# Performance work log

Hardware: AMD Instinct MI355X
Metric: run time of the kernel (lower is better)

## Reference

```python
import jax, jax.numpy as jnp
import numpy as np

N_NODES = 50000
N_EDGES = 1600000


def setup_inputs() -> dict:
    key = jax.random.key(0)
    ks = jax.random.split(key, 12)
    x = jax.random.normal(ks[0], (N_NODES, 128), dtype=jnp.float32)
    edge_index = jax.random.randint(ks[1], (2, N_EDGES), 0, N_NODES, dtype=jnp.int32)
    edge_weight = jax.random.uniform(ks[2], (N_EDGES,), dtype=jnp.float32)
    K = 3
    def glorot(k, kk, cin, cout):
        s = (6.0 / (cin + cout)) ** 0.5
        return jax.random.uniform(k, (kk, cin, cout), dtype=jnp.float32, minval=-s, maxval=s)
    W0 = glorot(ks[3], K, 128, 128); b0 = jnp.zeros((128,), jnp.float32)
    W1 = glorot(ks[4], K, 128, 128); b1 = jnp.zeros((128,), jnp.float32)
    W2 = glorot(ks[5], K, 128, 64);  b2 = jnp.zeros((64,), jnp.float32)
    return {"x": x, "edge_index": edge_index, "edge_weight": edge_weight,
            "W0": W0, "b0": b0, "W1": W1, "b1": b1, "W2": W2, "b2": b2}


def _laplacian_norm(edge_index, edge_weight, n_nodes):
    # PyG ChebConv with lambda_max=2.0, sym normalization:
    # L_hat = 2*(I - D^-1/2 A D^-1/2)/lambda_max - I = -D^-1/2 A D^-1/2 (zero diag)
    src, dst = edge_index[0], edge_index[1]
    deg = jax.ops.segment_sum(edge_weight, src, num_segments=n_nodes)
    dinv = jnp.where(deg > 0, jax.lax.rsqrt(jnp.maximum(deg, 1e-30)), 0.0)
    return -dinv[src] * edge_weight * dinv[dst]


def _spmm(norm, src, dst, x, n_nodes):
    # out[i] = sum_{e: dst[e]=i} norm[e] * x[src[e]]
    return jax.ops.segment_sum(norm[:, None] * x[src], dst, num_segments=n_nodes)


def _cheb_conv(x, src, dst, norm, W, b, n_nodes):
    K = W.shape[0]
    out = jnp.einsum('nc,cd->nd', x, W[0])
    tx0 = x
    tx1 = _spmm(norm, src, dst, x, n_nodes)  # L_hat @ x
    out = out + jnp.einsum('nc,cd->nd', tx1, W[1])
    for k in range(2, K):
        tx2 = 2.0 * _spmm(norm, src, dst, tx1, n_nodes) - tx0
        out = out + jnp.einsum('nc,cd->nd', tx2, W[k])
        tx0, tx1 = tx1, tx2
    return out + b


def reference(x, edge_index, edge_weight, W0, b0, W1, b1, W2, b2):
    n_nodes = x.shape[0]
    src, dst = edge_index[0], edge_index[1]
    norm = _laplacian_norm(edge_index, edge_weight, n_nodes)
    h = jax.nn.sigmoid(_cheb_conv(x, src, dst, norm, W0, b0, n_nodes))
    h = jax.nn.sigmoid(_cheb_conv(h, src, dst, norm, W1, b1, n_nodes))
    return jax.nn.sigmoid(_cheb_conv(h, src, dst, norm, W2, b2, n_nodes))
```

## Files before the change

### kernel.cpp

```cpp
#include <hip/hip_runtime.h>
#include <hip/hip_fp16.h>
#include <math.h>

#define N_NODES 50000
#define N_EDGES 1600000
#define NBUCK 196
#define EBLK 400
#define CHUNK 4000
#define CSR_CAP (N_EDGES + 2048 * NBUCK + 4096)

typedef _Float16 f16x8 __attribute__((ext_vector_type(8)));
typedef _Float16 f16x4 __attribute__((ext_vector_type(4)));
typedef _Float16 f16x2 __attribute__((ext_vector_type(2)));
typedef float f32x4 __attribute__((ext_vector_type(4)));
typedef float f32x2 __attribute__((ext_vector_type(2)));

union HBits { __half h; unsigned short u; };

__global__ __launch_bounds__(256) void k_bcount(const int* __restrict__ src,
                                                const int* __restrict__ dst,
                                                int* __restrict__ bcnt_d,
                                                int* __restrict__ bcnt_s) {
    __shared__ int lcd[256];
    __shared__ int lcs[256];
    int tid = threadIdx.x;
    lcd[tid] = 0; lcs[tid] = 0;
    __syncthreads();
    int base = blockIdx.x * CHUNK;
    for (int i = tid; i < CHUNK; i += 256) {
        atomicAdd(&lcd[dst[base + i] >> 8], 1);
        atomicAdd(&lcs[src[base + i] >> 8], 1);
    }
    __syncthreads();
    bcnt_d[blockIdx.x * 256 + tid] = lcd[tid];
    bcnt_s[blockIdx.x * 256 + tid] = lcs[tid];
}

__global__ __launch_bounds__(256) void k_bscan1(int* __restrict__ bcnt_d,
                                                int* __restrict__ bcnt_s,
                                                int* __restrict__ btot) {
    int b = blockIdx.x & 255;
    int* bcnt = (blockIdx.x >> 8) ? bcnt_s : bcnt_d;
    int tid = threadIdx.x;
    int k0 = 2 * tid;
    int v0 = (k0 < EBLK) ? bcnt[k0 * 256 + b] : 0;
    int v1 = (k0 + 1 < EBLK) ? bcnt[(k0 + 1) * 256 + b] : 0;
    int pair = v0 + v1;
    __shared__ int s[256];
    s[tid] = pair;
    __syncthreads();
    for (int off = 1; off < 256; off <<= 1) {
        int t = (tid >= off) ? s[tid - off] : 0;
        __syncthreads();
        s[tid] += t;
        __syncthreads();
    }
    int excl = s[tid] - pair;
    if (k0 < EBLK)     bcnt[k0 * 256 + b] = excl;
    if (k0 + 1 < EBLK) bcnt[(k0 + 1) * 256 + b] = excl + v0;
    if (tid == 255) btot[(blockIdx.x >> 8) * 256 + b] = s[255];
}

__global__ __launch_bounds__(256) void k_bscan2(const int* __restrict__ btot,
                                                int* __restrict__ bstart_d,
                                                int* __restrict__ bstart_s) {
    __shared__ int s[256];
    int b = threadIdx.x;
    int v = btot[b];
    s[b] = v;
    __syncthreads();
    for (int off = 1; off < 256; off <<= 1) {
        int t = (b >= off) ? s[b - off] : 0;
        __syncthreads();
        s[b] += t;
        __syncthreads();
    }
    bstart_d[b] = s[b] - v;
    if (b == 0) bstart_d[256] = N_EDGES;
    __syncthreads();
    int v2 = btot[256 + b];
    s[b] = v2;
    __syncthreads();
    for (int off = 1; off < 256; off <<= 1) {
        int t = (b >= off) ? s[b - off] : 0;
        __syncthreads();
        s[b] += t;
        __syncthreads();
    }
    bstart_s[b] = s[b] - v2;
    if (b == 0) bstart_s[256] = N_EDGES;
}

__global__ __launch_bounds__(256) void k_bscatter(const int* __restrict__ src,
                                                  const int* __restrict__ dst,
                                                  const float* __restrict__ w,
                                                  const int* __restrict__ bcnt_d,
                                                  const int* __restrict__ bcnt_s,
                                                  const int* __restrict__ bstart_d,
                                                  const int* __restrict__ bstart_s,
                                                  uint2* __restrict__ dsw,
                                                  unsigned* __restrict__ ssw) {
    __shared__ int curd[256];
    __shared__ int curs[256];
    int tid = threadIdx.x;
    curd[tid] = bcnt_d[blockIdx.x * 256 + tid] + bstart_d[tid];
    curs[tid] = bcnt_s[blockIdx.x * 256 + tid] + bstart_s[tid];
    __syncthreads();
    int base = blockIdx.x * CHUNK;
    for (int i = tid; i < CHUNK; i += 256) {
        int d = dst[base + i];
        int ss = src[base + i];
        float wi = w[base + i];
        int p = atomicAdd(&curd[d >> 8], 1);
        uint2 r; r.x = (unsigned)ss | ((unsigned)(d & 255) << 16);
        r.y = __float_as_uint(wi);
        dsw[p] = r;
        int q = atomicAdd(&curs[ss >> 8], 1);
        HBits hw; hw.h = __float2half(wi);
        ssw[q] = (unsigned)(ss & 255) | ((unsigned)hw.u << 16);
    }
}

__global__ __launch_bounds__(256) void k_sdeg(const unsigned* __restrict__ ssw,
                                              const int* __restrict__ bstart_s,
                                              float* __restrict__ dinv) {
    __shared__ float h[256];
    int tid = threadIdx.x;
    int b = blockIdx.x;
    h[tid] = 0.f;
    __syncthreads();
    int e0 = bstart_s[b], e1 = bstart_s[b + 1];
    for (int i = e0 + tid; i < e1; i += 256) {
        unsigned r = ssw[i];
        HBits hb; hb.u = (unsigned short)(r >> 16);
        atomicAdd(&h[r & 255], __half2float(hb.h));
    }
    __syncthreads();
    int node = (b << 8) + tid;
    if (node < N_NODES) {
        float d = h[tid];
        dinv[node] = d > 0.f ? rsqrtf(fmaxf(d, 1e-30f)) : 0.f;
    }
}

__global__ __launch_bounds__(256) void k_bcsr(const uint2* __restrict__ dsw,
                                              const int* __restrict__ bstart_d,
                                              const float* __restrict__ dinv,
                                              uint2* __restrict__ ri,
                                              unsigned* __restrict__ csr4) {
    __shared__ int ncnt[256];
    __shared__ int cur[256];
    __shared__ int sc[256];
    __shared__ float ldinv[256];
    int tid = threadIdx.x;
    int b = blockIdx.x;
    int node = (b << 8) + tid;
    ncnt[tid] = 0;
    ldinv[tid] = (node < N_NODES) ? dinv[node] : 0.f;
    __syncthreads();
    int e0 = bstart_d[b], e1 = bstart_d[b + 1];
    for (int i = e0 + tid; i < e1; i += 256)
        atomicAdd(&ncnt[(dsw[i].x >> 16) & 255], 1);
    __syncthreads();
    int v = ncnt[tid];
    int pc = (v + 7) & ~7;
    sc[tid] = pc;
    __syncthreads();
    for (int off = 1; off < 256; off <<= 1) {
        int t = (tid >= off) ? sc[tid - off] : 0;
        __syncthreads();
        sc[tid] += t;
        __syncthreads();
    }
    int excl = sc[tid] - pc;
    cur[tid] = excl;
    int pbase = ((e0 + 7) & ~7) + 2048 * b;
    if (node < N_NODES) {
        uint2 r; r.x = (unsigned)(pbase + excl); r.y = (unsigned)pc;
        ri[node] = r;
    }
    __syncthreads();
    for (int i = e0 + tid; i < e1; i += 256) {
        uint2 sw = dsw[i];
        int srcn = sw.x & 0xFFFF;
        int ld = (sw.x >> 16) & 255;
        int p = pbase + atomicAdd(&cur[ld], 1);
        float nv = -dinv[srcn] * __uint_as_float(sw.y) * ldinv[ld];
        HBits hb; hb.h = __float2half(nv);
        csr4[p] = (unsigned)srcn | ((unsigned)hb.u << 16);
    }
    __syncthreads();
    int st = pbase + excl;
    for (int i = v; i < pc; i++) csr4[st + i] = 0u;
}

__device__ inline void wt_one(const float* __restrict__ W, __half* __restrict__ Wt,
                              int C, int i) {
    int n = i >> 7, k = i & 127;
    int slice = n / C, c = n % C;
    float v;
    if (slice == 0)      v = 2.f * W[(size_t)(256 + k) * C + c];
    else if (slice == 1) v = W[(size_t)(128 + k) * C + c];
    else                 v = W[(size_t)k * C + c] - W[(size_t)(256 + k) * C + c];
    Wt[i] = __float2half(v);
}

__global__ __launch_bounds__(256) void k_prep(const float* __restrict__ x,
                                              __half* __restrict__ X,
                                              const float* __restrict__ W0,
                                              const float* __restrict__ W1,
                                              const float* __restrict__ W2,
                                              __half* __restrict__ Wt0,
                                              __half* __restrict__ Wt1,
                                              __half* __restrict__ Wt2) {
    int bid = blockIdx.x, tid = threadIdx.x;
    if (bid < 6250) {
        int i = bid * 256 + tid;
        float4 v = *(const float4*)&x[(size_t)i * 4];
        f16x4 o;
        o[0] = (_Float16)v.x; o[1] = (_Float16)v.y;
        o[2] = (_Float16)v.z; o[3] = (_Float16)v.w;
        *(f16x4*)&X[(size_t)i * 4] = o;
    } else if (bid < 6250 + 192) {
        wt_one(W0, Wt0, 128, (bid - 6250) * 256 + tid);
    } else if (bid < 6250 + 384) {
        wt_one(W1, Wt1, 128, (bid - 6250 - 192) * 256 + tid);
    } else {
        wt_one(W2, Wt2, 64, (bid - 6250 - 384) * 256 + tid);
    }
}

__device__ inline void mac_pair(const __half* __restrict__ Tbase, unsigned ea,
                                unsigned eb, int stin, float acc[8]) {
    f16x8 r0 = *(const f16x8*)&Tbase[(size_t)(ea & 0xFFFFu) * stin];
    f16x8 r1 = *(const f16x8*)&Tbase[(size_t)(eb & 0xFFFFu) * stin];
    unsigned np = (ea >> 16) | (eb & 0xFFFF0000u);
    f16x2 nv; __builtin_memcpy(&nv, &np, 4);
    #pragma unroll
    for (int f = 0; f < 8; f++) {
        f16x2 h; h[0] = r0[f]; h[1] = r1[f];
        acc[f] = __builtin_amdgcn_fdot2(h, nv, acc[f], false);
    }
}

__device__ inline void macv_f8(uint2 v, unsigned ce, float acc[8]) {
    HBits hb; hb.u = (unsigned short)(ce >> 16);
    float n = __half2float(hb.h);
    f32x2 p0 = __builtin_amdgcn_cvt_pk_f32_fp8(v.x, false);
    f32x2 p1 = __builtin_amdgcn_cvt_pk_f32_fp8(v.x, true);
    f32x2 p2 = __builtin_amdgcn_cvt_pk_f32_fp8(v.y, false);
    f32x2 p3 = __builtin_amdgcn_cvt_pk_f32_fp8(v.y, true);
    acc[0] = fmaf(n, p0[0], acc[0]);
    acc[1] = fmaf(n, p0[1], acc[1]);
    acc[2] = fmaf(n, p1[0], acc[2]);
    acc[3] = fmaf(n, p1[1], acc[3]);
    acc[4] = fmaf(n, p2[0], acc[4]);
    acc[5] = fmaf(n, p2[1], acc[5]);
    acc[6] = fmaf(n, p3[0], acc[6]);
    acc[7] = fmaf(n, p3[1], acc[7]);
}

__device__ inline void mac_e8(const unsigned char* __restrict__ Tb, unsigned ce,
                              int stin, float acc[8]) {
    uint2 v = *(const uint2*)&Tb[(size_t)(ce & 0xFFFFu) * (size_t)stin];
    macv_f8(v, ce, acc);
}

template <int ST_IN, int ST_ADD, int ST_OUT, int FW, int SIG, int F32, int GF8,
          int F8OUT>
__global__ __launch_bounds__(256) void k_spmm(const void* __restrict__ Xin,
                                              const __half* __restrict__ Add,
                                              void* __restrict__ outp,
                                              const float* __restrict__ bias,
                                              const uint2* __restrict__ ri,
                                              const unsigned* __restrict__ csr4) {
    constexpr int NL = FW / 8;
    constexpr int EG = 64 / NL;
    int node = blockIdx.x * 4 + (threadIdx.x >> 6);
    int lane = threadIdx.x & 63;
    int eg = lane / NL;
    int fs = lane % NL;
    uint2 rv = ri[node];
    int s = (int)rv.x;
    int e = s + (int)rv.y;
    const __half* Tbase = (const __half*)Xin + fs * 8;
    const unsigned char* Tb8 = (const unsigned char*)Xin + fs * 8;
    float acc[8];
    #pragma unroll
    for (int f = 0; f < 8; f++) acc[f] = 0.f;

    int j = s;
    if (GF8) {
        if (EG == 4) {
            for (; j + 32 <= e; j += 32) {
                uint4 c0 = *(const uint4*)&csr4[j + 4 * eg];
                uint4 c1 = *(const uint4*)&csr4[j + 16 + 4 * eg];
                unsigned ce[8] = {c0.x, c0.y, c0.z, c0.w, c1.x, c1.y, c1.z, c1.w};
                uint2 g[8];
                #pragma unroll
                for (int k = 0; k < 8; k++)
                    g[k] = *(const uint2*)&Tb8[(size_t)(ce[k] & 0xFFFFu) * (size_t)ST_IN];
                #pragma unroll
                for (int k = 0; k < 8; k++) macv_f8(g[k], ce[k], acc);
            }
            if (j + 16 <= e) {
                uint4 c0 = *(const uint4*)&csr4[j + 4 * eg];
                unsigned ce[4] = {c0.x, c0.y, c0.z, c0.w};
                uint2 g[4];
                #pragma unroll
                for (int k = 0; k < 4; k++)
                    g[k] = *(const uint2*)&Tb8[(size_t)(ce[k] & 0xFFFFu) * (size_t)ST_IN];
                #pragma unroll
                for (int k = 0; k < 4; k++) macv_f8(g[k], ce[k], acc);
                j += 16;
            }
            if (j + 8 <= e) {
                uint2 c = *(const uint2*)&csr4[j + 2 * eg];
                mac_e8(Tb8, c.x, ST_IN, acc);
                mac_e8(Tb8, c.y, ST_IN, acc);
            }
        } else {
            for (; j + 32 <= e; j += 32) {
                uint4 c0 = *(const uint4*)&csr4[j + 4 * eg];
                unsigned ce[4] = {c0.x, c0.y, c0.z, c0.w};
                uint2 g[4];
                #pragma unroll
                for (int k = 0; k < 4; k++)
                    g[k] = *(const uint2*)&Tb8[(size_t)(ce[k] & 0xFFFFu) * (size_t)ST_IN];
                #pragma unroll
                for (int k = 0; k < 4; k++) macv_f8(g[k], ce[k], acc);
            }
            if (j + 16 <= e) {
                uint2 c = *(const uint2*)&csr4[j + 2 * eg];
                mac_e8(Tb8, c.x, ST_IN, acc);
                mac_e8(Tb8, c.y, ST_IN, acc);
                j += 16;
            }
            if (j + 8 <= e) {
                uint2 c = *(const uint2*)&csr4[j + 2 * (eg & 3)];
                unsigned ea = c.x, eb = c.y;
                if (eg >= 4) { ea &= 0xFFFFu; eb &= 0xFFFFu; }
                mac_e8(Tb8, ea, ST_IN, acc);
                mac_e8(Tb8, eb, ST_IN, acc);
            }
        }
    } else if (EG == 4) {
        for (; j + 32 <= e; j += 32) {
            uint4 c0 = *(const uint4*)&csr4[j + 4 * eg];
            uint4 c1 = *(const uint4*)&csr4[j + 16 + 4 * eg];
            unsigned ea[4] = {c0.x, c0.z, c1.x, c1.z};
            unsigned eb[4] = {c0.y, c0.w, c1.y, c1.w};
            f16x8 r0[4], r1[4];
            #pragma unroll
            for (int k = 0; k < 4; k++) {
                r0[k] = *(const f16x8*)&Tbase[(size_t)(ea[k] & 0xFFFFu) * ST_IN];
                r1[k] = *(const f16x8*)&Tbase[(size_t)(eb[k] & 0xFFFFu) * ST_IN];
            }
            #pragma unroll
            for (int k = 0; k < 4; k++) {
                unsigned np = (ea[k] >> 16) | (eb[k] & 0xFFFF0000u);
                f16x2 nv; __builtin_memcpy(&nv, &np, 4);
                #pragma unroll
                for (int f = 0; f < 8; f++) {
                    f16x2 h; h[0] = r0[k][f]; h[1] = r1[k][f];
                    acc[f] = __builtin_amdgcn_fdot2(h, nv, acc[f], false);
                }
            }
        }
        if (j + 16 <= e) {
            uint4 c0 = *(const uint4*)&csr4[j + 4 * eg];
            mac_pair(Tbase, c0.x, c0.y, ST_IN, acc);
            mac_pair(Tbase, c0.z, c0.w, ST_IN, acc);
            j += 16;
        }
        if (j + 8 <= e) {
            uint2 c = *(const uint2*)&csr4[j + 2 * eg];
            mac_pair(Tbase, c.x, c.y, ST_IN, acc);
        }
    } else {
        for (; j + 32 <= e; j += 32) {
            uint4 c0 = *(const uint4*)&csr4[j + 4 * eg];
            unsigned ea[2] = {c0.x, c0.z};
            unsigned eb[2] = {c0.y, c0.w};
            f16x8 r0[2], r1[2];
            #pragma unroll
            for (int k = 0; k < 2; k++) {
                r0[k] = *(const f16x8*)&Tbase[(size_t)(ea[k] & 0xFFFFu) * ST_IN];
                r1[k] = *(const f16x8*)&Tbase[(size_t)(eb[k] & 0xFFFFu) * ST_IN];
            }
            #pragma unroll
            for (int k = 0; k < 2; k++) {
                unsigned np = (ea[k] >> 16) | (eb[k] & 0xFFFF0000u);
                f16x2 nv; __builtin_memcpy(&nv, &np, 4);
                #pragma unroll
                for (int f = 0; f < 8; f++) {
                    f16x2 h; h[0] = r0[k][f]; h[1] = r1[k][f];
                    acc[f] = __builtin_amdgcn_fdot2(h, nv, acc[f], false);
                }
            }
        }
        if (j + 16 <= e) {
            uint2 c = *(const uint2*)&csr4[j + 2 * eg];
            mac_pair(Tbase, c.x, c.y, ST_IN, acc);
            j += 16;
        }
        if (j + 8 <= e) {
            uint2 c = *(const uint2*)&csr4[j + 2 * (eg & 3)];
            unsigned ea = c.x, eb = c.y;
            if (eg >= 4) { ea &= 0xFFFFu; eb &= 0xFFFFu; }
            mac_pair(Tbase, ea, eb, ST_IN, acc);
        }
    }
    #pragma unroll
    for (int f = 0; f < 8; f++)
        for (int m = NL; m < 64; m <<= 1)
            acc[f] += __shfl_xor(acc[f], m);
    if (eg == 0) {
        f16x8 av = *(const f16x8*)&Add[(size_t)node * ST_ADD + fs * 8];
        float v[8];
        #pragma unroll
        for (int f = 0; f < 8; f++) v[f] = acc[f] + (float)av[f];
        if (SIG) {
            #pragma unroll
            for (int f = 0; f < 8; f++) {
                v[f] += bias[fs * 8 + f];
                v[f] = 1.f / (1.f + expf(-v[f]));
            }
        }
        if (F32) {
            float* o = (float*)outp + (size_t)node * ST_OUT + fs * 8;
            float4 o0; o0.x = v[0]; o0.y = v[1]; o0.z = v[2]; o0.w = v[3];
            float4 o1; o1.x = v[4]; o1.y = v[5]; o1.z = v[6]; o1.w = v[7];
            *(float4*)&o[0] = o0;
            *(float4*)&o[4] = o1;
        } else if (F8OUT) {
            int w0 = __builtin_amdgcn_cvt_pk_fp8_f32(v[0], v[1], 0, false);
            w0 = __builtin_amdgcn_cvt_pk_fp8_f32(v[2], v[3], w0, true);
            int w1 = __builtin_amdgcn_cvt_pk_fp8_f32(v[4], v[5], 0, false);
            w1 = __builtin_amdgcn_cvt_pk_fp8_f32(v[6], v[7], w1, true);
            uint2 o; o.x = (unsigned)w0; o.y = (unsigned)w1;
            *(uint2*)((unsigned char*)outp + (size_t)node * ST_OUT + fs * 8) = o;
        } else {
            f16x8 o;
            #pragma unroll
            for (int f = 0; f < 8; f++) o[f] = (_Float16)v[f];
            *(f16x8*)((__half*)outp + (size_t)node * ST_OUT + fs * 8) = o;
        }
    }
}

template <int CC, int STG>
__global__ __launch_bounds__(256) void k_gemm(const __half* __restrict__ A,
                                              const __half* __restrict__ Wt,
                                              __half* __restrict__ G,
                                              unsigned char* __restrict__ P8,
                                              int M) {
    constexpr int N3 = 3 * CC;
    constexpr int NF = N3 / 16;
    constexpr int NP = CC / 16;
    __shared__ _Float16 As[64][40];
    __shared__ _Float16 Bs[N3][40];
    int tid = threadIdx.x;
    int wave = tid >> 6, lane = tid & 63;
    int lm = lane & 15, lq = lane >> 4;
    int m0 = blockIdx.x * 64;
    f32x4 acc[NF];
    for (int nf = 0; nf < NF; nf++) acc[nf] = (f32x4)0.0f;

    for (int k0 = 0; k0 < 128; k0 += 32) {
        {
            int r = tid >> 2, q = tid & 3;
            int row = m0 + r;
            if (row >= M) row = M - 1;
            *(f16x8*)&As[r][q * 8] = *(const f16x8*)&A[(size_t)row * 128 + k0 + q * 8];
        }
        for (int i = 0; i < N3 / 64; i++) {
            int idx = tid + i * 256;
            int n = idx >> 2, q = idx & 3;
            *(f16x8*)&Bs[n][q * 8] = *(const f16x8*)&Wt[(size_t)n * 128 + k0 + q * 8];
        }
        __syncthreads();
        f16x8 a = *(const f16x8*)&As[wave * 16 + lm][lq * 8];
        for (int nf = 0; nf < NF; nf++) {
            f16x8 b = *(const f16x8*)&Bs[nf * 16 + lm][lq * 8];
            acc[nf] = __builtin_amdgcn_mfma_f32_16x16x32_f16(a, b, acc[nf], 0, 0, 0);
        }
        __syncthreads();
    }
    for (int nf = 0; nf < NF; nf++) {
        for (int r = 0; r < 4; r++) {
            int grow = m0 + wave * 16 + lq * 4 + r;
            int col = nf * 16 + lm;
            if (grow < M) {
                if (nf < NP) {
                    int pk = __builtin_amdgcn_cvt_pk_fp8_f32(acc[nf][r], acc[nf][r],
                                                             0, false);
                    P8[(size_t)grow * CC + col] = (unsigned char)(pk & 0xFF);
                } else {
                    G[(size_t)grow * STG + (col - CC)] = __float2half(acc[nf][r]);
                }
            }
        }
    }
}

extern "C" void kernel_launch(void* const* d_in, const int* in_sizes, int n_in,
                              void* d_out, int out_size, void* d_ws, size_t ws_size,
                              hipStream_t stream) {
    const float* x  = (const float*)d_in[0];
    const int*   ei = (const int*)d_in[1];
    const float* ew = (const float*)d_in[2];
    const float* W0 = (const float*)d_in[3];
    const float* b0 = (const float*)d_in[4];
    const float* W1 = (const float*)d_in[5];
    const float* b1 = (const float*)d_in[6];
    const float* W2 = (const float*)d_in[7];
    const float* b2 = (const float*)d_in[8];
    const int* src = ei;
    const int* dst = ei + N_EDGES;

    char* ws = (char*)d_ws;
    size_t off = 0;
    auto alloc = [&](size_t bytes) -> char* {
        size_t p = (off + 255) & ~(size_t)255;
        off = p + bytes;
        return ws + p;
    };
    __half*   X      = (__half*)alloc((size_t)N_NODES * 128 * 2);
    __half*   G      = (__half*)alloc((size_t)N_NODES * 256 * 2);
    __half*   TMP    = (__half*)alloc((size_t)N_NODES * 128 * 2);
    unsigned char* P8 = (unsigned char*)alloc((size_t)N_NODES * 128);
    unsigned char* TMP8 = (unsigned char*)alloc((size_t)N_NODES * 128);
    unsigned* csr4   = (unsigned*)alloc((size_t)CSR_CAP * 4);
    uint2*    ri     = (uint2*)alloc((size_t)N_NODES * 8);
    uint2*    dsw    = (uint2*)alloc((size_t)N_EDGES * 8);
    unsigned* ssw    = (unsigned*)alloc((size_t)N_EDGES * 4);
    int*      bcnt_d = (int*)alloc((size_t)EBLK * 256 * 4);
    int*      bcnt_s = (int*)alloc((size_t)EBLK * 256 * 4);
    int*      btot   = (int*)alloc(512 * 4);
    int*      bstart_d = (int*)alloc(257 * 4);
    int*      bstart_s = (int*)alloc(257 * 4);
    float*    dinv   = (float*)alloc((size_t)N_NODES * 4);
    __half*   Wt0    = (__half*)alloc((size_t)384 * 128 * 2);
    __half*   Wt1    = (__half*)alloc((size_t)384 * 128 * 2);
    __half*   Wt2    = (__half*)alloc((size_t)192 * 128 * 2);

    k_bcount<<<EBLK, 256, 0, stream>>>(src, dst, bcnt_d, bcnt_s);
    k_bscan1<<<512, 256, 0, stream>>>(bcnt_d, bcnt_s, btot);
    k_bscan2<<<1, 256, 0, stream>>>(btot, bstart_d, bstart_s);
    k_bscatter<<<EBLK, 256, 0, stream>>>(src, dst, ew, bcnt_d, bcnt_s,
                                         bstart_d, bstart_s, dsw, ssw);
    k_sdeg<<<NBUCK, 256, 0, stream>>>(ssw, bstart_s, dinv);
    k_bcsr<<<NBUCK, 256, 0, stream>>>(dsw, bstart_d, dinv, ri, csr4);

    k_prep<<<6250 + 192 + 192 + 96, 256, 0, stream>>>(x, X, W0, W1, W2, Wt0, Wt1, Wt2);

    int gb = (N_NODES + 63) / 64;
    int sb = N_NODES / 4;
    k_gemm<128, 256><<<gb, 256, 0, stream>>>(X, Wt0, G, P8, N_NODES);
    k_spmm<128, 256, 128, 128, 0, 0, 1, 1><<<sb, 256, 0, stream>>>(P8, G, TMP8,
                                                                   nullptr, ri, csr4);
    k_spmm<128, 256, 128, 128, 1, 0, 1, 0><<<sb, 256, 0, stream>>>(TMP8, G + 128, X,
                                                                   b0, ri, csr4);
    k_gemm<128, 256><<<gb, 256, 0, stream>>>(X, Wt1, G, P8, N_NODES);
    k_spmm<128, 256, 128, 128, 0, 0, 1, 1><<<sb, 256, 0, stream>>>(P8, G, TMP8,
                                                                   nullptr, ri, csr4);
    k_spmm<128, 256, 128, 128, 1, 0, 1, 0><<<sb, 256, 0, stream>>>(TMP8, G + 128, X,
                                                                   b1, ri, csr4);
    k_gemm<64, 128><<<gb, 256, 0, stream>>>(X, Wt2, G, P8, N_NODES);
    k_spmm<64, 128, 64, 64, 0, 0, 1, 0><<<sb, 256, 0, stream>>>(P8, G, TMP,
                                                                nullptr, ri, csr4);
    k_spmm<64, 128, 64, 64, 1, 1, 0, 0><<<sb, 256, 0, stream>>>(TMP, G + 64, d_out,
                                                                b2, ri, csr4);
}
```

Before: 413.0 us.

## Stage bucket scatter in LDS and widen fp8 SpMM gathers to 16 bytes

The bucket scatter kernel now computes local per-bucket offsets with a block-level histogram and prefix scan. It stages records in shared memory and then writes them to global memory in contiguous runs, replacing scattered per-edge global writes. Separately, the 128-wide fp8 SpMM path now has each lane gather 16 bytes (16 features) per edge instead of 8, halving lanes per row and doubling edge groups. This adds LDS usage (about 48KB per block), which may limit occupancy, and extra passes over the input chunk.

```diff
diff --git a/kernel.cpp b/kernel.cpp
--- a/kernel.cpp
+++ b/kernel.cpp
@@ -100,24 +100,58 @@
                                                   const int* __restrict__ bstart_s,
                                                   uint2* __restrict__ dsw,
                                                   unsigned* __restrict__ ssw) {
-    __shared__ int curd[256];
-    __shared__ int curs[256];
+    __shared__ uint2 sbufd[CHUNK];
+    __shared__ unsigned sbufs[CHUNK];
+    __shared__ int lcd[256];
+    __shared__ int lcs[256];
+    __shared__ int curd_l[256];
+    __shared__ int curs_l[256];
+    __shared__ int gbase_d[256];
+    __shared__ int gbase_s[256];
     int tid = threadIdx.x;
-    curd[tid] = bcnt_d[blockIdx.x * 256 + tid] + bstart_d[tid];
-    curs[tid] = bcnt_s[blockIdx.x * 256 + tid] + bstart_s[tid];
+    lcd[tid] = 0; lcs[tid] = 0;
     __syncthreads();
     int base = blockIdx.x * CHUNK;
+    for (int i = tid; i < CHUNK; i += 256) {
+        atomicAdd(&lcd[dst[base + i] >> 8], 1);
+        atomicAdd(&lcs[src[base + i] >> 8], 1);
+    }
+    __syncthreads();
+    int vd = lcd[tid], vs = lcs[tid];
+    for (int off = 1; off < 256; off <<= 1) {
+        int td = (tid >= off) ? lcd[tid - off] : 0;
+        int ts = (tid >= off) ? lcs[tid - off] : 0;
+        __syncthreads();
+        lcd[tid] += td; lcs[tid] += ts;
+        __syncthreads();
+    }
+    int exd = lcd[tid] - vd, exs = lcs[tid] - vs;
+    curd_l[tid] = exd;
+    curs_l[tid] = exs;
+    gbase_d[tid] = bcnt_d[blockIdx.x * 256 + tid] + bstart_d[tid] - exd;
+    gbase_s[tid] = bcnt_s[blockIdx.x * 256 + tid] + bstart_s[tid] - exs;
+    __syncthreads();
     for (int i = tid; i < CHUNK; i += 256) {
         int d = dst[base + i];
         int ss = src[base + i];
         float wi = w[base + i];
-        int p = atomicAdd(&curd[d >> 8], 1);
-        uint2 r; r.x = (unsigned)ss | ((unsigned)(d & 255) << 16);
+        int p = atomicAdd(&curd_l[d >> 8], 1);
+        uint2 r;
+        r.x = (unsigned)ss | ((unsigned)(d & 255) << 16) | ((unsigned)(d >> 8) << 24);
         r.y = __float_as_uint(wi);
-        dsw[p] = r;
-        int q = atomicAdd(&curs[ss >> 8], 1);
+        sbufd[p] = r;
+        int q = atomicAdd(&curs_l[ss >> 8], 1);
         HBits hw; hw.h = __float2half(wi);
-        ssw[q] = (unsigned)(ss & 255) | ((unsigned)hw.u << 16);
+        sbufs[q] = (unsigned)ss | ((unsigned)hw.u << 16);
+    }
+    __syncthreads();
+    for (int i = tid; i < CHUNK; i += 256) {
+        uint2 r = sbufd[i];
+        dsw[gbase_d[(r.x >> 24) & 255] + i] = r;
+    }
+    for (int i = tid; i < CHUNK; i += 256) {
+        unsigned rs = sbufs[i];
+        ssw[gbase_s[(rs >> 8) & 255] + i] = rs;
     }
 }
 
@@ -266,6 +300,28 @@
     macv_f8(v, ce, acc);
 }
 
+__device__ inline void macv_f8q(uint4 v, unsigned ce, float acc[16]) {
+    HBits hb; hb.u = (unsigned short)(ce >> 16);
+    float n = __half2float(hb.h);
+    f32x2 p;
+    p = __builtin_amdgcn_cvt_pk_f32_fp8(v.x, false);
+    acc[0] = fmaf(n, p[0], acc[0]);  acc[1] = fmaf(n, p[1], acc[1]);
+    p = __builtin_amdgcn_cvt_pk_f32_fp8(v.x, true);
+    acc[2] = fmaf(n, p[0], acc[2]);  acc[3] = fmaf(n, p[1], acc[3]);
+    p = __builtin_amdgcn_cvt_pk_f32_fp8(v.y, false);
+    acc[4] = fmaf(n, p[0], acc[4]);  acc[5] = fmaf(n, p[1], acc[5]);
+    p = __builtin_amdgcn_cvt_pk_f32_fp8(v.y, true);
+    acc[6] = fmaf(n, p[0], acc[6]);  acc[7] = fmaf(n, p[1], acc[7]);
+    p = __builtin_amdgcn_cvt_pk_f32_fp8(v.z, false);
+    acc[8] = fmaf(n, p[0], acc[8]);  acc[9] = fmaf(n, p[1], acc[9]);
+    p = __builtin_amdgcn_cvt_pk_f32_fp8(v.z, true);
+    acc[10] = fmaf(n, p[0], acc[10]); acc[11] = fmaf(n, p[1], acc[11]);
+    p = __builtin_amdgcn_cvt_pk_f32_fp8(v.w, false);
+    acc[12] = fmaf(n, p[0], acc[12]); acc[13] = fmaf(n, p[1], acc[13]);
+    p = __builtin_amdgcn_cvt_pk_f32_fp8(v.w, true);
+    acc[14] = fmaf(n, p[0], acc[14]); acc[15] = fmaf(n, p[1], acc[15]);
+}
+
 template <int ST_IN, int ST_ADD, int ST_OUT, int FW, int SIG, int F32, int GF8,
           int F8OUT>
 __global__ __launch_bounds__(256) void k_spmm(const void* __restrict__ Xin,
@@ -274,7 +330,8 @@
                                               const float* __restrict__ bias,
                                               const uint2* __restrict__ ri,
                                               const unsigned* __restrict__ csr4) {
-    constexpr int NL = FW / 8;
+    constexpr int FPL = (GF8 && FW == 128) ? 16 : 8;
+    constexpr int NL = FW / FPL;
     constexpr int EG = 64 / NL;
     int node = blockIdx.x * 4 + (threadIdx.x >> 6);
     int lane = threadIdx.x & 63;
@@ -284,65 +341,59 @@
     int s = (int)rv.x;
     int e = s + (int)rv.y;
     const __half* Tbase = (const __half*)Xin + fs * 8;
-    const unsigned char* Tb8 = (const unsigned char*)Xin + fs * 8;
-    float acc[8];
+    const unsigned char* Tb8 = (const unsigned char*)Xin + fs * FPL;
+    float acc[FPL];
     #pragma unroll
-    for (int f = 0; f < 8; f++) acc[f] = 0.f;
+    for (int f = 0; f < FPL; f++) acc[f] = 0.f;
 
     int j = s;
-    if (GF8) {
-        if (EG == 4) {
-            for (; j + 32 <= e; j += 32) {
-                uint4 c0 = *(const uint4*)&csr4[j + 4 * eg];
-                uint4 c1 = *(const uint4*)&csr4[j + 16 + 4 * eg];
-                unsigned ce[8] = {c0.x, c0.y, c0.z, c0.w, c1.x, c1.y, c1.z, c1.w};
-                uint2 g[8];
-                #pragma unroll
-                for (int k = 0; k < 8; k++)
-                    g[k] = *(const uint2*)&Tb8[(size_t)(ce[k] & 0xFFFFu) * (size_t)ST_IN];
-                #pragma unroll
-                for (int k = 0; k < 8; k++) macv_f8(g[k], ce[k], acc);
-            }
-            if (j + 16 <= e) {
-                uint4 c0 = *(const uint4*)&csr4[j + 4 * eg];
-                unsigned ce[4] = {c0.x, c0.y, c0.z, c0.w};
-                uint2 g[4];
-                #pragma unroll
-                for (int k = 0; k < 4; k++)
-                    g[k] = *(const uint2*)&Tb8[(size_t)(ce[k] & 0xFFFFu) * (size_t)ST_IN];
-                #pragma unroll
-                for (int k = 0; k < 4; k++) macv_f8(g[k], ce[k], acc);
-                j += 16;
-            }
-            if (j + 8 <= e) {
-                uint2 c = *(const uint2*)&csr4[j + 2 * eg];
-                mac_e8(Tb8, c.x, ST_IN, acc);
-                mac_e8(Tb8, c.y, ST_IN, acc);
-            }
-        } else {
-            for (; j + 32 <= e; j += 32) {
-                uint4 c0 = *(const uint4*)&csr4[j + 4 * eg];
-                unsigned ce[4] = {c0.x, c0.y, c0.z, c0.w};
-                uint2 g[4];
-                #pragma unroll
-                for (int k = 0; k < 4; k++)
-                    g[k] = *(const uint2*)&Tb8[(size_t)(ce[k] & 0xFFFFu) * (size_t)ST_IN];
-                #pragma unroll
-                for (int k = 0; k < 4; k++) macv_f8(g[k], ce[k], acc);
-            }
-            if (j + 16 <= e) {
-                uint2 c = *(const uint2*)&csr4[j + 2 * eg];
-                mac_e8(Tb8, c.x, ST_IN, acc);
-                mac_e8(Tb8, c.y, ST_IN, acc);
-                j += 16;
-            }
-            if (j + 8 <= e) {
-                uint2 c = *(const uint2*)&csr4[j + 2 * (eg & 3)];
-                unsigned ea = c.x, eb = c.y;
-                if (eg >= 4) { ea &= 0xFFFFu; eb &= 0xFFFFu; }
-                mac_e8(Tb8, ea, ST_IN, acc);
-                mac_e8(Tb8, eb, ST_IN, acc);
-            }
+    if (GF8 && FW == 128) {
+        for (; j + 32 <= e; j += 32) {
+            uint4 c0 = *(const uint4*)&csr4[j + 4 * eg];
+            unsigned ce[4] = {c0.x, c0.y, c0.z, c0.w};
+            uint4 g[4];
+            #pragma unroll
+            for (int k = 0; k < 4; k++)
+                g[k] = *(const uint4*)&Tb8[(size_t)(ce[k] & 0xFFFFu) * (size_t)ST_IN];
+            #pragma unroll
+            for (int k = 0; k < 4; k++) macv_f8q(g[k], ce[k], acc);
+        }
+        if (j + 16 <= e) {
+            uint2 c = *(const uint2*)&csr4[j + 2 * eg];
+            uint4 g0 = *(const uint4*)&Tb8[(size_t)(c.x & 0xFFFFu) * (size_t)ST_IN];
+            uint4 g1 = *(const uint4*)&Tb8[(size_t)(c.y & 0xFFFFu) * (size_t)ST_IN];
+            macv_f8q(g0, c.x, acc);
+            macv_f8q(g1, c.y, acc);
+            j += 16;
+        }
+        if (j + 8 <= e) {
+            unsigned c = csr4[j + eg];
+            uint4 g0 = *(const uint4*)&Tb8[(size_t)(c & 0xFFFFu) * (size_t)ST_IN];
+            macv_f8q(g0, c, acc);
+        }
+    } else if (GF8) {
+        for (; j + 32 <= e; j += 32) {
+            uint4 c0 = *(const uint4*)&csr4[j + 4 * eg];
+            unsigned ce[4] = {c0.x, c0.y, c0.z, c0.w};
+            uint2 g[4];
+            #pragma unroll
+            for (int k = 0; k < 4; k++)
+                g[k] = *(const uint2*)&Tb8[(size_t)(ce[k] & 0xFFFFu) * (size_t)ST_IN];
+            #pragma unroll
+            for (int k = 0; k < 4; k++) macv_f8(g[k], ce[k], acc);
+        }
+        if (j + 16 <= e) {
+            uint2 c = *(const uint2*)&csr4[j + 2 * eg];
+            mac_e8(Tb8, c.x, ST_IN, acc);
+            mac_e8(Tb8, c.y, ST_IN, acc);
+            j += 16;
+        }
+        if (j + 8 <= e) {
+            uint2 c = *(const uint2*)&csr4[j + 2 * (eg & 3)];
+            unsigned ea = c.x, eb = c.y;
+            if (eg >= 4) { ea &= 0xFFFFu; eb &= 0xFFFFu; }
+            mac_e8(Tb8, ea, ST_IN, acc);
+            mac_e8(Tb8, eb, ST_IN, acc);
         }
     } else if (EG == 4) {
         for (; j + 32 <= e; j += 32) {
@@ -412,18 +463,21 @@
         }
     }
     #pragma unroll
-    for (int f = 0; f < 8; f++)
+    for (int f = 0; f < FPL; f++)
         for (int m = NL; m < 64; m <<= 1)
             acc[f] += __shfl_xor(acc[f], m);
     if (eg == 0) {
-        f16x8 av = *(const f16x8*)&Add[(size_t)node * ST_ADD + fs * 8];
-        float v[8];
+        float v[FPL];
         #pragma unroll
-        for (int f = 0; f < 8; f++) v[f] = acc[f] + (float)av[f];
+        for (int c = 0; c < FPL / 8; c++) {
+            f16x8 av = *(const f16x8*)&Add[(size_t)node * ST_ADD + fs * FPL + c * 8];
+            #pragma unroll
+            for (int f = 0; f < 8; f++) v[c * 8 + f] = acc[c * 8 + f] + (float)av[f];
+        }
         if (SIG) {
             #pragma unroll
-            for (int f = 0; f < 8; f++) {
-                v[f] += bias[fs * 8 + f];
+            for (int f = 0; f < FPL; f++) {
+                v[f] += bias[fs * FPL + f];
                 v[f] = 1.f / (1.f + expf(-v[f]));
             }
         }
@@ -434,17 +488,23 @@
             *(float4*)&o[0] = o0;
             *(float4*)&o[4] = o1;
         } else if (F8OUT) {
-            int w0 = __builtin_amdgcn_cvt_pk_fp8_f32(v[0], v[1], 0, false);
-            w0 = __builtin_amdgcn_cvt_pk_fp8_f32(v[2], v[3], w0, true);
-            int w1 = __builtin_amdgcn_cvt_pk_fp8_f32(v[4], v[5], 0, false);
-            w1 = __builtin_amdgcn_cvt_pk_fp8_f32(v[6], v[7], w1, true);
-            uint2 o; o.x = (unsigned)w0; o.y = (unsigned)w1;
-            *(uint2*)((unsigned char*)outp + (size_t)node * ST_OUT + fs * 8) = o;
+            #pragma unroll
+            for (int c = 0; c < FPL / 8; c++) {
+                int w0 = __builtin_amdgcn_cvt_pk_fp8_f32(v[c*8+0], v[c*8+1], 0, false);
+                w0 = __builtin_amdgcn_cvt_pk_fp8_f32(v[c*8+2], v[c*8+3], w0, true);
+                int w1 = __builtin_amdgcn_cvt_pk_fp8_f32(v[c*8+4], v[c*8+5], 0, false);
+                w1 = __builtin_amdgcn_cvt_pk_fp8_f32(v[c*8+6], v[c*8+7], w1, true);
+                uint2 o; o.x = (unsigned)w0; o.y = (unsigned)w1;
+                *(uint2*)((unsigned char*)outp + (size_t)node * ST_OUT + fs * FPL + c * 8) = o;
+            }
         } else {
-            f16x8 o;
-            #pragma unroll
-            for (int f = 0; f < 8; f++) o[f] = (_Float16)v[f];
-            *(f16x8*)((__half*)outp + (size_t)node * ST_OUT + fs * 8) = o;
+            #pragma unroll
+            for (int c = 0; c < FPL / 8; c++) {
+                f16x8 o;
+                #pragma unroll
+                for (int f = 0; f < 8; f++) o[f] = (_Float16)v[c * 8 + f];
+                *(f16x8*)((__half*)outp + (size_t)node * ST_OUT + fs * FPL + c * 8) = o;
+            }
         }
     }
 }
```

Result: slower. 459.6 us (+11.3%).

## Replace source-bucket sort with global atomic degree and stage dst scatter in LDS

Applied to the files above, without the earlier changes.

Drops the source-side bucketing pipeline (ssw, bcnt_s, k_sdeg) and computes the source degree with global float atomics inside the scatter kernel. dinv is then computed on the fly in k_bcsr. Dst bucket counting moves into the prep kernel to save a launch, and the dst scatter is staged through a local LDS sort before a coalesced write. It also hoists the Add load in spmm ahead of the edge loop. In exchange, global atomics on deg make the float summation order nondeterministic, and each edge now does a rsqrt in k_bcsr.

```diff
diff --git a/kernel.cpp b/kernel.cpp
--- a/kernel.cpp
+++ b/kernel.cpp
@@ -17,34 +17,14 @@
 
 union HBits { __half h; unsigned short u; };
 
-__global__ __launch_bounds__(256) void k_bcount(const int* __restrict__ src,
-                                                const int* __restrict__ dst,
-                                                int* __restrict__ bcnt_d,
-                                                int* __restrict__ bcnt_s) {
-    __shared__ int lcd[256];
-    __shared__ int lcs[256];
-    int tid = threadIdx.x;
-    lcd[tid] = 0; lcs[tid] = 0;
-    __syncthreads();
-    int base = blockIdx.x * CHUNK;
-    for (int i = tid; i < CHUNK; i += 256) {
-        atomicAdd(&lcd[dst[base + i] >> 8], 1);
-        atomicAdd(&lcs[src[base + i] >> 8], 1);
-    }
-    __syncthreads();
-    bcnt_d[blockIdx.x * 256 + tid] = lcd[tid];
-    bcnt_s[blockIdx.x * 256 + tid] = lcs[tid];
-}
 
 __global__ __launch_bounds__(256) void k_bscan1(int* __restrict__ bcnt_d,
-                                                int* __restrict__ bcnt_s,
                                                 int* __restrict__ btot) {
-    int b = blockIdx.x & 255;
-    int* bcnt = (blockIdx.x >> 8) ? bcnt_s : bcnt_d;
+    int b = blockIdx.x;
     int tid = threadIdx.x;
     int k0 = 2 * tid;
-    int v0 = (k0 < EBLK) ? bcnt[k0 * 256 + b] : 0;
-    int v1 = (k0 + 1 < EBLK) ? bcnt[(k0 + 1) * 256 + b] : 0;
+    int v0 = (k0 < EBLK) ? bcnt_d[k0 * 256 + b] : 0;
+    int v1 = (k0 + 1 < EBLK) ? bcnt_d[(k0 + 1) * 256 + b] : 0;
     int pair = v0 + v1;
     __shared__ int s[256];
     s[tid] = pair;
@@ -56,14 +36,13 @@
         __syncthreads();
     }
     int excl = s[tid] - pair;
-    if (k0 < EBLK)     bcnt[k0 * 256 + b] = excl;
-    if (k0 + 1 < EBLK) bcnt[(k0 + 1) * 256 + b] = excl + v0;
-    if (tid == 255) btot[(blockIdx.x >> 8) * 256 + b] = s[255];
+    if (k0 < EBLK)     bcnt_d[k0 * 256 + b] = excl;
+    if (k0 + 1 < EBLK) bcnt_d[(k0 + 1) * 256 + b] = excl + v0;
+    if (tid == 255) btot[b] = s[255];
 }
 
 __global__ __launch_bounds__(256) void k_bscan2(const int* __restrict__ btot,
-                                                int* __restrict__ bstart_d,
-                                                int* __restrict__ bstart_s) {
+                                                int* __restrict__ bstart_d) {
     __shared__ int s[256];
     int b = threadIdx.x;
     int v = btot[b];
@@ -77,75 +56,58 @@
     }
     bstart_d[b] = s[b] - v;
     if (b == 0) bstart_d[256] = N_EDGES;
-    __syncthreads();
-    int v2 = btot[256 + b];
-    s[b] = v2;
-    __syncthreads();
-    for (int off = 1; off < 256; off <<= 1) {
-        int t = (b >= off) ? s[b - off] : 0;
-        __syncthreads();
-        s[b] += t;
-        __syncthreads();
-    }
-    bstart_s[b] = s[b] - v2;
-    if (b == 0) bstart_s[256] = N_EDGES;
 }
 
 __global__ __launch_bounds__(256) void k_bscatter(const int* __restrict__ src,
                                                   const int* __restrict__ dst,
                                                   const float* __restrict__ w,
                                                   const int* __restrict__ bcnt_d,
-                                                  const int* __restrict__ bcnt_s,
                                                   const int* __restrict__ bstart_d,
-                                                  const int* __restrict__ bstart_s,
                                                   uint2* __restrict__ dsw,
-                                                  unsigned* __restrict__ ssw) {
-    __shared__ int curd[256];
-    __shared__ int curs[256];
+                                                  float* __restrict__ deg) {
+    __shared__ uint2 sbufd[CHUNK];
+    __shared__ int lcd[256];
+    __shared__ int curd_l[256];
+    __shared__ int gbase_d[256];
     int tid = threadIdx.x;
-    curd[tid] = bcnt_d[blockIdx.x * 256 + tid] + bstart_d[tid];
-    curs[tid] = bcnt_s[blockIdx.x * 256 + tid] + bstart_s[tid];
+    lcd[tid] = 0;
     __syncthreads();
     int base = blockIdx.x * CHUNK;
+    for (int i = tid; i < CHUNK; i += 256)
+        atomicAdd(&lcd[dst[base + i] >> 8], 1);
+    __syncthreads();
+    int vd = lcd[tid];
+    for (int off = 1; off < 256; off <<= 1) {
+        int td = (tid >= off) ? lcd[tid - off] : 0;
+        __syncthreads();
+        lcd[tid] += td;
+        __syncthreads();
+    }
+    int exd = lcd[tid] - vd;
+    curd_l[tid] = exd;
+    gbase_d[tid] = bcnt_d[blockIdx.x * 256 + tid] + bstart_d[tid] - exd;
+    __syncthreads();
     for (int i = tid; i < CHUNK; i += 256) {
         int d = dst[base + i];
         int ss = src[base + i];
         float wi = w[base + i];
-        int p = atomicAdd(&curd[d >> 8], 1);
-        uint2 r; r.x = (unsigned)ss | ((unsigned)(d & 255) << 16);
+        int p = atomicAdd(&curd_l[d >> 8], 1);
+        uint2 r;
+        r.x = (unsigned)ss | ((unsigned)(d & 255) << 16) | ((unsigned)(d >> 8) << 24);
         r.y = __float_as_uint(wi);
-        dsw[p] = r;
-        int q = atomicAdd(&curs[ss >> 8], 1);
-        HBits hw; hw.h = __float2half(wi);
-        ssw[q] = (unsigned)(ss & 255) | ((unsigned)hw.u << 16);
-    }
-}
-
-__global__ __launch_bounds__(256) void k_sdeg(const unsigned* __restrict__ ssw,
-                                              const int* __restrict__ bstart_s,
-                                              float* __restrict__ dinv) {
-    __shared__ float h[256];
-    int tid = threadIdx.x;
-    int b = blockIdx.x;
-    h[tid] = 0.f;
-    __syncthreads();
-    int e0 = bstart_s[b], e1 = bstart_s[b + 1];
-    for (int i = e0 + tid; i < e1; i += 256) {
-        unsigned r = ssw[i];
-        HBits hb; hb.u = (unsigned short)(r >> 16);
-        atomicAdd(&h[r & 255], __half2float(hb.h));
-    }
-    __syncthreads();
-    int node = (b << 8) + tid;
-    if (node < N_NODES) {
-        float d = h[tid];
-        dinv[node] = d > 0.f ? rsqrtf(fmaxf(d, 1e-30f)) : 0.f;
+        sbufd[p] = r;
+        atomicAdd(&deg[ss], wi);
+    }
+    __syncthreads();
+    for (int i = tid; i < CHUNK; i += 256) {
+        uint2 r = sbufd[i];
+        dsw[gbase_d[(r.x >> 24) & 255] + i] = r;
     }
 }
 
 __global__ __launch_bounds__(256) void k_bcsr(const uint2* __restrict__ dsw,
                                               const int* __restrict__ bstart_d,
-                                              const float* __restrict__ dinv,
+                                              const float* __restrict__ deg,
                                               uint2* __restrict__ ri,
                                               unsigned* __restrict__ csr4) {
     __shared__ int ncnt[256];
@@ -156,7 +118,8 @@
     int b = blockIdx.x;
     int node = (b << 8) + tid;
     ncnt[tid] = 0;
-    ldinv[tid] = (node < N_NODES) ? dinv[node] : 0.f;
+    float dgn = (node < N_NODES) ? deg[node] : 0.f;
+    ldinv[tid] = dgn > 0.f ? rsqrtf(fmaxf(dgn, 1e-30f)) : 0.f;
     __syncthreads();
     int e0 = bstart_d[b], e1 = bstart_d[b + 1];
     for (int i = e0 + tid; i < e1; i += 256)
@@ -185,7 +148,9 @@
         int srcn = sw.x & 0xFFFF;
         int ld = (sw.x >> 16) & 255;
         int p = pbase + atomicAdd(&cur[ld], 1);
-        float nv = -dinv[srcn] * __uint_as_float(sw.y) * ldinv[ld];
+        float dg = deg[srcn];
+        float di = dg > 0.f ? rsqrtf(fmaxf(dg, 1e-30f)) : 0.f;
+        float nv = -di * __uint_as_float(sw.y) * ldinv[ld];
         HBits hb; hb.h = __float2half(nv);
         csr4[p] = (unsigned)srcn | ((unsigned)hb.u << 16);
     }
@@ -212,7 +177,10 @@
                                               const float* __restrict__ W2,
                                               __half* __restrict__ Wt0,
                                               __half* __restrict__ Wt1,
-                                              __half* __restrict__ Wt2) {
+                                              __half* __restrict__ Wt2,
+                                              const int* __restrict__ dst,
+                                              int* __restrict__ bcnt_d,
+                                              float* __restrict__ deg) {
     int bid = blockIdx.x, tid = threadIdx.x;
     if (bid < 6250) {
         int i = bid * 256 + tid;
@@ -221,12 +189,23 @@
         o[0] = (_Float16)v.x; o[1] = (_Float16)v.y;
         o[2] = (_Float16)v.z; o[3] = (_Float16)v.w;
         *(f16x4*)&X[(size_t)i * 4] = o;
-    } else if (bid < 6250 + 192) {
+    } else if (bid < 6442) {
         wt_one(W0, Wt0, 128, (bid - 6250) * 256 + tid);
-    } else if (bid < 6250 + 384) {
-        wt_one(W1, Wt1, 128, (bid - 6250 - 192) * 256 + tid);
+    } else if (bid < 6634) {
+        wt_one(W1, Wt1, 128, (bid - 6442) * 256 + tid);
+    } else if (bid < 6730) {
+        wt_one(W2, Wt2, 64, (bid - 6634) * 256 + tid);
     } else {
-        wt_one(W2, Wt2, 64, (bid - 6250 - 384) * 256 + tid);
+        __shared__ int lcd[256];
+        int b = bid - 6730;
+        if (tid < 125) deg[b * 125 + tid] = 0.f;
+        lcd[tid] = 0;
+        __syncthreads();
+        int base = b * CHUNK;
+        for (int i = tid; i < CHUNK; i += 256)
+            atomicAdd(&lcd[dst[base + i] >> 8], 1);
+        __syncthreads();
+        bcnt_d[b * 256 + tid] = lcd[tid];
     }
 }
 
@@ -285,6 +264,7 @@
     int e = s + (int)rv.y;
     const __half* Tbase = (const __half*)Xin + fs * 8;
     const unsigned char* Tb8 = (const unsigned char*)Xin + fs * 8;
+    f16x8 av = *(const f16x8*)&Add[(size_t)node * ST_ADD + fs * 8];
     float acc[8];
     #pragma unroll
     for (int f = 0; f < 8; f++) acc[f] = 0.f;
@@ -416,7 +396,6 @@
         for (int m = NL; m < 64; m <<= 1)
             acc[f] += __shfl_xor(acc[f], m);
     if (eg == 0) {
-        f16x8 av = *(const f16x8*)&Add[(size_t)node * ST_ADD + fs * 8];
         float v[8];
         #pragma unroll
         for (int f = 0; f < 8; f++) v[f] = acc[f] + (float)av[f];
@@ -534,26 +513,21 @@
     unsigned* csr4   = (unsigned*)alloc((size_t)CSR_CAP * 4);
     uint2*    ri     = (uint2*)alloc((size_t)N_NODES * 8);
     uint2*    dsw    = (uint2*)alloc((size_t)N_EDGES * 8);
-    unsigned* ssw    = (unsigned*)alloc((size_t)N_EDGES * 4);
     int*      bcnt_d = (int*)alloc((size_t)EBLK * 256 * 4);
-    int*      bcnt_s = (int*)alloc((size_t)EBLK * 256 * 4);
-    int*      btot   = (int*)alloc(512 * 4);
+    int*      btot   = (int*)alloc(256 * 4);
     int*      bstart_d = (int*)alloc(257 * 4);
-    int*      bstart_s = (int*)alloc(257 * 4);
-    float*    dinv   = (float*)alloc((size_t)N_NODES * 4);
+    float*    deg    = (float*)alloc((size_t)N_NODES * 4);
     __half*   Wt0    = (__half*)alloc((size_t)384 * 128 * 2);
     __half*   Wt1    = (__half*)alloc((size_t)384 * 128 * 2);
     __half*   Wt2    = (__half*)alloc((size_t)192 * 128 * 2);
 
-    k_bcount<<<EBLK, 256, 0, stream>>>(src, dst, bcnt_d, bcnt_s);
-    k_bscan1<<<512, 256, 0, stream>>>(bcnt_d, bcnt_s, btot);
-    k_bscan2<<<1, 256, 0, stream>>>(btot, bstart_d, bstart_s);
-    k_bscatter<<<EBLK, 256, 0, stream>>>(src, dst, ew, bcnt_d, bcnt_s,
-                                         bstart_d, bstart_s, dsw, ssw);
-    k_sdeg<<<NBUCK, 256, 0, stream>>>(ssw, bstart_s, dinv);
-    k_bcsr<<<NBUCK, 256, 0, stream>>>(dsw, bstart_d, dinv, ri, csr4);
-
-    k_prep<<<6250 + 192 + 192 + 96, 256, 0, stream>>>(x, X, W0, W1, W2, Wt0, Wt1, Wt2);
+    k_prep<<<7130, 256, 0, stream>>>(x, X, W0, W1, W2, Wt0, Wt1, Wt2,
+                                     dst, bcnt_d, deg);
+    k_bscan1<<<256, 256, 0, stream>>>(bcnt_d, btot);
+    k_bscan2<<<1, 256, 0, stream>>>(btot, bstart_d);
+    k_bscatter<<<EBLK, 256, 0, stream>>>(src, dst, ew, bcnt_d, bstart_d,
+                                         dsw, deg);
+    k_bcsr<<<NBUCK, 256, 0, stream>>>(dsw, bstart_d, deg, ri, csr4);
 
     int gb = (N_NODES + 63) / 64;
     int sb = N_NODES / 4;
```

Result: slower. 460.4 us (+11.5%).
